# Kernel optimization log

Hardware: AMD Instinct MI355X
Metric: run time of the kernel (lower is better)

Reference implementation:

```python
import jax, jax.numpy as jnp
import numpy as np

ORDER = 2
C_IN = 32
C_OUT = 32
SUPPORT_LEN = 2


def setup_inputs() -> dict:
    key = jax.random.key(0)
    k1, k2, k3, k4 = jax.random.split(key, 4)
    B, C, V, L = 32, C_IN, 2048, 12
    x = jax.random.normal(k1, (B, C, V, L), dtype=jnp.float32)
    supports = jax.random.uniform(k2, (SUPPORT_LEN, V, V), dtype=jnp.float32) / V
    c_cat = (ORDER * SUPPORT_LEN + 1) * C_IN
    W = jax.random.normal(k3, (C_OUT, c_cat), dtype=jnp.float32) * (1.0 / np.sqrt(c_cat))
    b = jax.random.normal(k4, (C_OUT,), dtype=jnp.float32) * 0.01
    return {"x": x, "supports": supports, "W": W, "b": b}


def reference(x, supports, W, b):
    # x: [B, C, V, L]; supports: [S, V, V]; W: [c_out, (order*S+1)*C]; b: [c_out]
    out = [x]
    for s in range(supports.shape[0]):  # fixed small S
        A = supports[s]
        x1 = jnp.einsum('bcvl,vw->bcwl', x, A)
        out.append(x1)
        for _ in range(ORDER - 1):
            x1 = jnp.einsum('bcvl,vw->bcwl', x1, A)
            out.append(x1)
    h = jnp.concatenate(out, axis=1)  # [B, (order*S+1)*C, V, L]
    # 1x1 conv == channel-mixing matmul; dropout is identity in eval mode
    y = jnp.einsum('bcvl,oc->bovl', h, W) + b[None, :, None, None]
    return y
```

## Files before the change

### kernel.cpp

```cpp
#include <hip/hip_runtime.h>

#define BB 32
#define CC 32
#define VV 2048
#define LL 12
#define NCOL 12288
#define MMEGA 8192

typedef __attribute__((ext_vector_type(8))) short bf16x8;
typedef __attribute__((ext_vector_type(4))) float f32x4;

__device__ __forceinline__ unsigned short f2b(float f) {
    union { float f; unsigned u; } v; v.f = f;
    unsigned u = v.u;
    unsigned r = (u + 0x7fffu + ((u >> 16) & 1u)) >> 16;
    return (unsigned short)r;
}
__device__ __forceinline__ float b2f(unsigned short h) {
    union { unsigned u; float f; } v; v.u = ((unsigned)h) << 16;
    return v.f;
}

__device__ __forceinline__ void stg(const unsigned short* g, unsigned short* l) {
    __builtin_amdgcn_global_load_lds((const __attribute__((address_space(1))) void*)g,
                                     (__attribute__((address_space(3))) void*)l, 16, 0, 0);
}

__global__ void k_prepA(const float* __restrict__ A,
                        unsigned short* __restrict__ Abf,
                        unsigned short* __restrict__ Gt) {
    __shared__ float t[32][33];
    const int s = blockIdx.z;
    const float* As = A + (size_t)s * VV * VV;
    const int w0 = blockIdx.x * 32, v0 = blockIdx.y * 32;
    const int tid = threadIdx.x;
    const int cc = tid & 31;
    unsigned short* Ao = Abf + (size_t)s * VV * VV;
#pragma unroll
    for (int i = 0; i < 4; i++) {
        int rr = (tid >> 5) + i * 8;
        float val = As[(size_t)(v0 + rr) * VV + w0 + cc];
        t[rr][cc] = val;
        Ao[(size_t)(v0 + rr) * VV + w0 + cc] = f2b(val);
    }
    __syncthreads();
    unsigned short* G = Gt + (size_t)(2 * s) * VV * VV;
#pragma unroll
    for (int i = 0; i < 4; i++) {
        int rr = (tid >> 5) + i * 8;
        G[(size_t)(w0 + rr) * VV + v0 + cc] = f2b(t[cc][rr]);
    }
}

__global__ void k_transpose_x(const float* __restrict__ x,
                              unsigned short* __restrict__ Xb) {
    __shared__ float t[128 * 13];
    const int bc = blockIdx.y;
    const int v0 = blockIdx.x * 128;
    const float* xs = x + (size_t)bc * VV * LL + (size_t)v0 * LL;
    const int tid = threadIdx.x;
#pragma unroll
    for (int i = 0; i < 6; i++) {
        int e = tid + i * 256;
        int col = e / 12, row = e - col * 12;
        t[col * 13 + row] = xs[e];
    }
    __syncthreads();
    unsigned short* X = Xb + (size_t)bc * LL * VV + v0;
#pragma unroll
    for (int i = 0; i < 2; i++) {
        int flat = tid + i * 256;
        if (flat < 384) {
            int row = flat >> 5;
            int col = (flat & 31) * 4;
            ushort4 o;
            o.x = f2b(t[(col + 0) * 13 + row]);
            o.y = f2b(t[(col + 1) * 13 + row]);
            o.z = f2b(t[(col + 2) * 13 + row]);
            o.w = f2b(t[(col + 3) * 13 + row]);
            *(ushort4*)&X[(size_t)row * VV + col] = o;
        }
    }
}

__global__ __launch_bounds__(512, 2) void k_gemm8(
    const unsigned short* __restrict__ Ag, const unsigned short* __restrict__ Bg,
    unsigned short* __restrict__ Cg, int K, int ldc,
    size_t aStr, size_t bStr, size_t cStr)
{
    __shared__ unsigned short SH[65536];
    const int tid  = threadIdx.x;
    const int lane = tid & 63;
    const int wid  = tid >> 6;
    const int wr   = wid >> 2;
    const int wc   = wid & 3;
    const int fr   = lane & 15;
    const int g    = lane >> 4;
    const int NT   = K >> 6;

    const int m0 = blockIdx.y * 256;
    const int n0 = blockIdx.x * 256;
    const unsigned short* gA = Ag + blockIdx.z * aStr + (size_t)m0 * K;
    const unsigned short* gB = Bg + blockIdx.z * bStr + (size_t)n0 * K;
    unsigned short* gC = Cg + blockIdx.z * cStr;

    const int lrow  = lane >> 3;
    const int lslot = (lane & 7) ^ lrow;
    const size_t laneGOff = (size_t)lrow * K + lslot * 8;

    const int qa  = wid * 16;
    const int rA0 = (qa & 63) + ((qa & 64) << 1);
    const int rA1 = ((qa + 8) & 63) + (((qa + 8) & 64) << 1);
    const int rB0 = (qa & 31) + ((qa & ~31) << 1);
    const int rB1 = ((qa + 8) & 31) + (((qa + 8) & ~31) << 1);

    const int frlow = fr & 7;
    const int sw0 = ((0 + g) ^ frlow) << 4;
    const int sw1 = ((4 + g) ^ frlow) << 4;
    const int aOffB = (wr * 128 + fr) * 128;
    const int bOffB = (wc * 64  + fr) * 128;

    f32x4 acc[8][4];
#pragma unroll
    for (int i = 0; i < 8; ++i)
#pragma unroll
        for (int j = 0; j < 4; ++j) { f32x4 z = {0.f, 0.f, 0.f, 0.f}; acc[i][j] = z; }

#define STG_A(Lb, rb, kt) stg(gA + (size_t)(rb) * K + ((size_t)(kt) << 6) + laneGOff, (Lb) + (rb) * 64)
#define STG_B(Lb, rb, kt) stg(gB + (size_t)(rb) * K + ((size_t)(kt) << 6) + laneGOff, (Lb) + (rb) * 64)
#define ST_Aa(Lb, kt) do { if ((kt) < NT) { STG_A(Lb, rA0, kt);      STG_A(Lb, rA1, kt);      } } while (0)
#define ST_Ab(Lb, kt) do { if ((kt) < NT) { STG_A(Lb, rA0 + 64, kt); STG_A(Lb, rA1 + 64, kt); } } while (0)
#define ST_Ba(Lb, kt) do { if ((kt) < NT) { STG_B(Lb, rB0, kt);      STG_B(Lb, rB1, kt);      } } while (0)
#define ST_Bb(Lb, kt) do { if ((kt) < NT) { STG_B(Lb, rB0 + 32, kt); STG_B(Lb, rB1 + 32, kt); } } while (0)
#define VM6() asm volatile("s_waitcnt vmcnt(6)" ::: "memory")
#define VM0() asm volatile("s_waitcnt vmcnt(0)" ::: "memory")
#define LGKM(n) asm volatile("s_waitcnt lgkmcnt(" #n ")" ::: "memory")
#define SCHB() __builtin_amdgcn_sched_barrier(0)
#define SBAR() __builtin_amdgcn_s_barrier()

    unsigned short* A0L = SH;
    unsigned short* B0L = SH + 16384;
    unsigned short* A1L = SH + 32768;
    unsigned short* B1L = SH + 49152;

    ST_Aa(A0L, 0); ST_Ab(A0L, 0); ST_Ba(B0L, 0); ST_Bb(B0L, 0);
    ST_Aa(A1L, 1); ST_Ab(A1L, 1); ST_Ba(B1L, 1);
    if (NT > 1) { VM6(); } else { VM0(); }
    SBAR();

    bf16x8 aA[4][2], aB[4][2], b0[2][2], b1[2][2];
    {
        const char* Ab = (const char*)SH;
        const char* Bb = Ab + 32768;
#pragma unroll
        for (int i = 0; i < 4; ++i) {
            aA[i][0] = *(const bf16x8*)(Ab + aOffB + i * 2048 + sw0);
            aA[i][1] = *(const bf16x8*)(Ab + aOffB + i * 2048 + sw1);
        }
#pragma unroll
        for (int j = 0; j < 2; ++j) {
            b0[j][0] = *(const bf16x8*)(Bb + bOffB + j * 2048 + sw0);
            b0[j][1] = *(const bf16x8*)(Bb + bOffB + j * 2048 + sw1);
        }
    }

    for (int t = 0; t < NT; ++t) {
        const char* Ab  = (const char*)(SH + ((t & 1) << 15));
        const char* Bb  = Ab + 32768;
        const char* AbN = (const char*)(SH + (((t + 1) & 1) << 15));
        const char* BbN = AbN + 32768;
        unsigned short* An = SH + (((t + 1) & 1) << 15);
        unsigned short* Bn = An + 16384;
        unsigned short* Ac = SH + ((t & 1) << 15);
        unsigned short* Bc = Ac + 16384;
        (void)An;

#pragma unroll
        for (int i = 0; i < 4; ++i) {
            aB[i][0] = *(const bf16x8*)(Ab + aOffB + 8192 + i * 2048 + sw0);
            aB[i][1] = *(const bf16x8*)(Ab + aOffB + 8192 + i * 2048 + sw1);
        }
        ST_Bb(Bn, t + 1);
        SBAR(); LGKM(8); SCHB();
        __builtin_amdgcn_s_setprio(1);
#pragma unroll
        for (int i = 0; i < 4; ++i)
#pragma unroll
            for (int j = 0; j < 2; ++j) {
                acc[i][j] = __builtin_amdgcn_mfma_f32_16x16x32_bf16(aA[i][0], b0[j][0], acc[i][j], 0, 0, 0);
                acc[i][j] = __builtin_amdgcn_mfma_f32_16x16x32_bf16(aA[i][1], b0[j][1], acc[i][j], 0, 0, 0);
            }
        __builtin_amdgcn_s_setprio(0);
        SBAR();

#pragma unroll
        for (int j = 0; j < 2; ++j) {
            b1[j][0] = *(const bf16x8*)(Bb + bOffB + 4096 + j * 2048 + sw0);
            b1[j][1] = *(const bf16x8*)(Bb + bOffB + 4096 + j * 2048 + sw1);
        }
        ST_Aa(Ac, t + 2);
        SBAR(); LGKM(4); SCHB();
        __builtin_amdgcn_s_setprio(1);
#pragma unroll
        for (int i = 0; i < 4; ++i)
#pragma unroll
            for (int j = 0; j < 2; ++j) {
                acc[4 + i][j] = __builtin_amdgcn_mfma_f32_16x16x32_bf16(aB[i][0], b0[j][0], acc[4 + i][j], 0, 0, 0);
                acc[4 + i][j] = __builtin_amdgcn_mfma_f32_16x16x32_bf16(aB[i][1], b0[j][1], acc[4 + i][j], 0, 0, 0);
            }
        __builtin_amdgcn_s_setprio(0);
        SBAR();

        ST_Ab(Ac, t + 2);
        SBAR(); LGKM(0); SCHB();
        __builtin_amdgcn_s_setprio(1);
#pragma unroll
        for (int i = 0; i < 4; ++i)
#pragma unroll
            for (int j = 0; j < 2; ++j) {
                acc[i][2 + j] = __builtin_amdgcn_mfma_f32_16x16x32_bf16(aA[i][0], b1[j][0], acc[i][2 + j], 0, 0, 0);
                acc[i][2 + j] = __builtin_amdgcn_mfma_f32_16x16x32_bf16(aA[i][1], b1[j][1], acc[i][2 + j], 0, 0, 0);
            }
        __builtin_amdgcn_s_setprio(0);
        SBAR();

        ST_Ba(Bc, t + 2);
        if (t + 2 < NT) { VM6(); } else { VM0(); }
        SBAR();
#pragma unroll
        for (int i = 0; i < 4; ++i) {
            aA[i][0] = *(const bf16x8*)(AbN + aOffB + i * 2048 + sw0);
            aA[i][1] = *(const bf16x8*)(AbN + aOffB + i * 2048 + sw1);
        }
#pragma unroll
        for (int j = 0; j < 2; ++j) {
            b0[j][0] = *(const bf16x8*)(BbN + bOffB + j * 2048 + sw0);
            b0[j][1] = *(const bf16x8*)(BbN + bOffB + j * 2048 + sw1);
        }
        LGKM(12); SCHB();
        __builtin_amdgcn_s_setprio(1);
#pragma unroll
        for (int i = 0; i < 4; ++i)
#pragma unroll
            for (int j = 0; j < 2; ++j) {
                acc[4 + i][2 + j] = __builtin_amdgcn_mfma_f32_16x16x32_bf16(aB[i][0], b1[j][0], acc[4 + i][2 + j], 0, 0, 0);
                acc[4 + i][2 + j] = __builtin_amdgcn_mfma_f32_16x16x32_bf16(aB[i][1], b1[j][1], acc[4 + i][2 + j], 0, 0, 0);
            }
        __builtin_amdgcn_s_setprio(0);
        SBAR();
    }

    const int er = g * 4;
#pragma unroll
    for (int i = 0; i < 8; ++i)
#pragma unroll
        for (int j = 0; j < 4; ++j) {
            int row = m0 + wr * 128 + i * 16 + er;
            int col = n0 + wc * 64 + j * 16 + fr;
#pragma unroll
            for (int r = 0; r < 4; ++r)
                gC[(size_t)(row + r) * ldc + col] = f2b(acc[i][j][r]);
        }
#undef STG_A
#undef STG_B
#undef ST_Aa
#undef ST_Ab
#undef ST_Ba
#undef ST_Bb
#undef VM6
#undef VM0
#undef LGKM
#undef SCHB
#undef SBAR
}

__global__ __launch_bounds__(192) void k_epilogue(const float* __restrict__ x,
                                                  const unsigned short* __restrict__ U,
                                                  const float* __restrict__ W,
                                                  const float* __restrict__ bias,
                                                  float* __restrict__ y) {
    __shared__ float xs[32][192];
    __shared__ unsigned short us[64][392];
    const int b = blockIdx.y;
    const int w0 = blockIdx.x * 16;
    const int tid = threadIdx.x;

    const float* xp = x + ((size_t)(b * 32) * VV + w0) * LL;
#pragma unroll 4
    for (int c = 0; c < 32; c++)
        xs[c][tid] = xp[(size_t)c * (VV * LL) + tid];

    {
        const int r0 = tid / 48;
        const int c0 = tid - r0 * 48;
#pragma unroll
        for (int it = 0; it < 16; ++it) {
            int r = it * 4 + r0;
            int krow = (r >> 4) * VV + w0 + (r & 15);
            const unsigned short* up = U + (size_t)krow * NCOL + b * 384 + c0 * 8;
            *(bf16x8*)&us[r][c0 * 8] = *(const bf16x8*)up;
        }
    }
    __syncthreads();

    const int w = tid / 12, l = tid - w * 12;
    float acc[32];
#pragma unroll
    for (int o = 0; o < 32; o++) acc[o] = bias[o];

    for (int c = 0; c < 32; c++) {
        float h = xs[c][tid];
#pragma unroll
        for (int o = 0; o < 32; o++) acc[o] += W[o * 160 + c] * h;
    }
    for (int c = 0; c < 32; c++) {
#pragma unroll
        for (int k = 0; k < 4; k++) {
            float h = b2f(us[k * 16 + w][c * 12 + l]);
#pragma unroll
            for (int o = 0; o < 32; o++) acc[o] += W[o * 160 + (k + 1) * 32 + c] * h;
        }
    }

    float* yp = y + ((size_t)(b * 32) * VV + w0) * LL;
#pragma unroll
    for (int o = 0; o < 32; o++)
        yp[(size_t)o * (VV * LL) + tid] = acc[o];
}

extern "C" void kernel_launch(void* const* d_in, const int* in_sizes, int n_in,
                              void* d_out, int out_size, void* d_ws, size_t ws_size,
                              hipStream_t stream) {
    const float* x        = (const float*)d_in[0];
    const float* supports = (const float*)d_in[1];
    const float* W        = (const float*)d_in[2];
    const float* bias     = (const float*)d_in[3];
    float* y = (float*)d_out;

    char* ws = (char*)d_ws;
    unsigned short* Xb  = (unsigned short*)(ws);
    unsigned short* Gt  = (unsigned short*)(ws + 50331648);
    unsigned short* Abf = (unsigned short*)(ws + 83886080);
    unsigned short* U   = (unsigned short*)(ws + 100663296);

    const size_t VB = (size_t)VV * VV;

    k_prepA<<<dim3(64, 64, 2), 256, 0, stream>>>(supports, Abf, Gt);

    k_gemm8<<<dim3(8, 8, 2), 512, 0, stream>>>(Gt, Abf, Gt + VB, VV, VV,
                                               2 * VB, VB, 2 * VB);

    k_transpose_x<<<dim3(16, 1024), 256, 0, stream>>>(x, Xb);

    k_gemm8<<<dim3(NCOL / 256, MMEGA / 256, 1), 512, 0, stream>>>(Gt, Xb, U, VV, NCOL,
                                                                  0, 0, 0);

    k_epilogue<<<dim3(VV / 16, BB), 192, 0, stream>>>(x, U, W, bias, y);
}
```

Baseline: 850.0 us.

## Split-K the small A² GEMM and remap mega-GEMM blocks across XCDs

The A·A GEMM (only 128 blocks) is split along K into two halves that write fp32 partials, followed by a combine kernel that sums them and converts to bf16. This doubles the block count to better fill the GPU's CUs. The large GEMM now uses a 1D grid with an XCD-aware block-to-tile mapping, so neighbouring tiles share L2 on the same chiplet. The split adds fp32 partial traffic and an extra kernel launch.

```diff
diff --git a/kernel.cpp b/kernel.cpp
--- a/kernel.cpp
+++ b/kernel.cpp
@@ -6,6 +6,7 @@
 #define LL 12
 #define NCOL 12288
 #define MMEGA 8192
+#define VB ((size_t)VV * VV)
 
 typedef __attribute__((ext_vector_type(8))) short bf16x8;
 typedef __attribute__((ext_vector_type(4))) float f32x4;
@@ -31,11 +32,11 @@
                         unsigned short* __restrict__ Gt) {
     __shared__ float t[32][33];
     const int s = blockIdx.z;
-    const float* As = A + (size_t)s * VV * VV;
+    const float* As = A + (size_t)s * VB;
     const int w0 = blockIdx.x * 32, v0 = blockIdx.y * 32;
     const int tid = threadIdx.x;
     const int cc = tid & 31;
-    unsigned short* Ao = Abf + (size_t)s * VV * VV;
+    unsigned short* Ao = Abf + (size_t)s * VB;
 #pragma unroll
     for (int i = 0; i < 4; i++) {
         int rr = (tid >> 5) + i * 8;
@@ -44,7 +45,7 @@
         Ao[(size_t)(v0 + rr) * VV + w0 + cc] = f2b(val);
     }
     __syncthreads();
-    unsigned short* G = Gt + (size_t)(2 * s) * VV * VV;
+    unsigned short* G = Gt + (size_t)(2 * s) * VB;
 #pragma unroll
     for (int i = 0; i < 4; i++) {
         int rr = (tid >> 5) + i * 8;
@@ -83,10 +84,12 @@
     }
 }
 
-__global__ __launch_bounds__(512, 2) void k_gemm8(
-    const unsigned short* __restrict__ Ag, const unsigned short* __restrict__ Bg,
-    unsigned short* __restrict__ Cg, int K, int ldc,
-    size_t aStr, size_t bStr, size_t cStr)
+template<bool F32OUT>
+__device__ __forceinline__ void gemm_core(const unsigned short* __restrict__ Ag,
+                                          const unsigned short* __restrict__ Bg,
+                                          void* __restrict__ Cg,
+                                          int ld, int Kloc, int koff,
+                                          int m0, int n0, int ldc)
 {
     __shared__ unsigned short SH[65536];
     const int tid  = threadIdx.x;
@@ -96,17 +99,14 @@
     const int wc   = wid & 3;
     const int fr   = lane & 15;
     const int g    = lane >> 4;
-    const int NT   = K >> 6;
-
-    const int m0 = blockIdx.y * 256;
-    const int n0 = blockIdx.x * 256;
-    const unsigned short* gA = Ag + blockIdx.z * aStr + (size_t)m0 * K;
-    const unsigned short* gB = Bg + blockIdx.z * bStr + (size_t)n0 * K;
-    unsigned short* gC = Cg + blockIdx.z * cStr;
+    const int NT   = Kloc >> 6;
+
+    const unsigned short* gA = Ag + (size_t)m0 * ld + koff;
+    const unsigned short* gB = Bg + (size_t)n0 * ld + koff;
 
     const int lrow  = lane >> 3;
     const int lslot = (lane & 7) ^ lrow;
-    const size_t laneGOff = (size_t)lrow * K + lslot * 8;
+    const size_t laneGOff = (size_t)lrow * ld + lslot * 8;
 
     const int qa  = wid * 16;
     const int rA0 = (qa & 63) + ((qa & 64) << 1);
@@ -126,8 +126,8 @@
 #pragma unroll
         for (int j = 0; j < 4; ++j) { f32x4 z = {0.f, 0.f, 0.f, 0.f}; acc[i][j] = z; }
 
-#define STG_A(Lb, rb, kt) stg(gA + (size_t)(rb) * K + ((size_t)(kt) << 6) + laneGOff, (Lb) + (rb) * 64)
-#define STG_B(Lb, rb, kt) stg(gB + (size_t)(rb) * K + ((size_t)(kt) << 6) + laneGOff, (Lb) + (rb) * 64)
+#define STG_A(Lb, rb, kt) stg(gA + (size_t)(rb) * ld + ((size_t)(kt) << 6) + laneGOff, (Lb) + (rb) * 64)
+#define STG_B(Lb, rb, kt) stg(gB + (size_t)(rb) * ld + ((size_t)(kt) << 6) + laneGOff, (Lb) + (rb) * 64)
 #define ST_Aa(Lb, kt) do { if ((kt) < NT) { STG_A(Lb, rA0, kt);      STG_A(Lb, rA1, kt);      } } while (0)
 #define ST_Ab(Lb, kt) do { if ((kt) < NT) { STG_A(Lb, rA0 + 64, kt); STG_A(Lb, rA1 + 64, kt); } } while (0)
 #define ST_Ba(Lb, kt) do { if ((kt) < NT) { STG_B(Lb, rB0, kt);      STG_B(Lb, rB1, kt);      } } while (0)
@@ -258,8 +258,12 @@
             int row = m0 + wr * 128 + i * 16 + er;
             int col = n0 + wc * 64 + j * 16 + fr;
 #pragma unroll
-            for (int r = 0; r < 4; ++r)
-                gC[(size_t)(row + r) * ldc + col] = f2b(acc[i][j][r]);
+            for (int r = 0; r < 4; ++r) {
+                if (F32OUT)
+                    ((float*)Cg)[(size_t)(row + r) * ldc + col] = acc[i][j][r];
+                else
+                    ((unsigned short*)Cg)[(size_t)(row + r) * ldc + col] = f2b(acc[i][j][r]);
+            }
         }
 #undef STG_A
 #undef STG_B
@@ -274,6 +278,47 @@
 #undef SBAR
 }
 
+__global__ __launch_bounds__(512, 2) void k_gemm_mega(
+    const unsigned short* __restrict__ Ag, const unsigned short* __restrict__ Bg,
+    unsigned short* __restrict__ Cg)
+{
+    const int bid = blockIdx.x;
+    const int xcd = bid & 7;
+    const int t   = bid >> 3;
+    const int sx  = t >> 5;
+    const int loc = t & 31;
+    const int x = sx * 8 + (loc & 7);
+    const int y = xcd * 4 + (loc >> 3);
+    gemm_core<false>(Ag, Bg, (void*)Cg, VV, VV, 0, y * 256, x * 256, NCOL);
+}
+
+__global__ __launch_bounds__(512, 2) void k_gemm_small(
+    const unsigned short* __restrict__ Gt, const unsigned short* __restrict__ Abf,
+    float* __restrict__ P)
+{
+    const int bid = blockIdx.x;
+    const int s  = bid >> 7;
+    const int kz = (bid >> 6) & 1;
+    const int y  = (bid >> 3) & 7;
+    const int x  = bid & 7;
+    const unsigned short* A = Gt + (size_t)(2 * s) * VB;
+    const unsigned short* B = Abf + (size_t)s * VB;
+    float* C = P + (size_t)(s * 2 + kz) * VB;
+    gemm_core<true>(A, B, (void*)C, VV, 1024, kz * 1024, y * 256, x * 256, VV);
+}
+
+__global__ void k_combine(const float* __restrict__ P,
+                          unsigned short* __restrict__ Gt) {
+    const int s = blockIdx.y;
+    size_t i = ((size_t)blockIdx.x * 256 + threadIdx.x) * 4;
+    float4 a = *(const float4*)(P + (size_t)(2 * s) * VB + i);
+    float4 b = *(const float4*)(P + (size_t)(2 * s + 1) * VB + i);
+    ushort4 o;
+    o.x = f2b(a.x + b.x); o.y = f2b(a.y + b.y);
+    o.z = f2b(a.z + b.z); o.w = f2b(a.w + b.w);
+    *(ushort4*)(Gt + (size_t)(2 * s + 1) * VB + i) = o;
+}
+
 __global__ __launch_bounds__(192) void k_epilogue(const float* __restrict__ x,
                                                   const unsigned short* __restrict__ U,
                                                   const float* __restrict__ W,
@@ -342,18 +387,17 @@
     unsigned short* Gt  = (unsigned short*)(ws + 50331648);
     unsigned short* Abf = (unsigned short*)(ws + 83886080);
     unsigned short* U   = (unsigned short*)(ws + 100663296);
-
-    const size_t VB = (size_t)VV * VV;
+    float*          P   = (float*)(ws + 100663296);
 
     k_prepA<<<dim3(64, 64, 2), 256, 0, stream>>>(supports, Abf, Gt);
 
-    k_gemm8<<<dim3(8, 8, 2), 512, 0, stream>>>(Gt, Abf, Gt + VB, VV, VV,
-                                               2 * VB, VB, 2 * VB);
+    k_gemm_small<<<dim3(256), 512, 0, stream>>>(Gt, Abf, P);
+
+    k_combine<<<dim3(4096, 2), 256, 0, stream>>>(P, Gt);
 
     k_transpose_x<<<dim3(16, 1024), 256, 0, stream>>>(x, Xb);
 
-    k_gemm8<<<dim3(NCOL / 256, MMEGA / 256, 1), 512, 0, stream>>>(Gt, Xb, U, VV, NCOL,
-                                                                  0, 0, 0);
+    k_gemm_mega<<<dim3(1536), 512, 0, stream>>>(Gt, Xb, U);
 
     k_epilogue<<<dim3(VV / 16, BB), 192, 0, stream>>>(x, U, W, bias, y);
 }
```

After: 833.7 us. Within noise of the previous version (-1.9%).
